# Performance work log

Hardware: AMD Instinct MI355X
Metric: run time of the kernel (lower is better)

Reference implementation:

```python
import jax, jax.numpy as jnp
import numpy as np

NUM_USERS = 100000
NUM_ITEMS = 50000
NUM_LAYERS = 4
DIM_H = 64
E_HALF = 2000000  # undirected interactions; symmetrized to 4M directed edges


def setup_inputs() -> dict:
    key = jax.random.key(0)
    k1, k2, k3, k4 = jax.random.split(key, 4)
    emb_users = 0.01 * jax.random.normal(k1, (NUM_USERS, DIM_H), dtype=jnp.float32)
    emb_items = 0.01 * jax.random.normal(k2, (NUM_ITEMS, DIM_H), dtype=jnp.float32)
    u = jax.random.randint(k3, (E_HALF,), 0, NUM_USERS, dtype=jnp.int64)
    it = jax.random.randint(k4, (E_HALF,), 0, NUM_ITEMS, dtype=jnp.int64) + NUM_USERS
    # bidirectional bipartite graph, as LightGCN expects
    src = jnp.concatenate([u, it])
    dst = jnp.concatenate([it, u])
    edge_index = jnp.stack([src, dst])  # [2, 4M]
    return {"emb_users": emb_users, "emb_items": emb_items, "edge_index": edge_index}


def reference(emb_users, emb_items, edge_index):
    N = emb_users.shape[0] + emb_items.shape[0]
    src, dst = edge_index[0], edge_index[1]
    # gcn_norm (add_self_loops=False): w_e = deg[src]^-1/2 * deg[dst]^-1/2
    deg = jax.ops.segment_sum(jnp.ones(src.shape[0], dtype=emb_users.dtype), dst, num_segments=N)
    dis = jnp.where(deg > 0, deg ** -0.5, 0.0).astype(emb_users.dtype)
    w = (dis[src] * dis[dst])[:, None]  # [E,1]

    emb = jnp.concatenate([emb_users, emb_items])  # [N, D]
    embs_sum = emb
    x = emb
    for _ in range(NUM_LAYERS):
        x = jax.ops.segment_sum(w * x[src], dst, num_segments=N)  # LGConv
        embs_sum = embs_sum + x
    # original: 1/(L+1) * mean over L+1 stacked layers -> sum / (L+1)^2
    emb_final = embs_sum / float((NUM_LAYERS + 1) ** 2)
    emb_users_final = emb_final[: emb_users.shape[0]]
    emb_items_final = emb_final[emb_users.shape[0]:]
    return (emb_users_final, emb_users, emb_items_final, emb_items)
```

## Files before the change

kernel.cpp:

```cpp
#include <hip/hip_runtime.h>
#include <hip/hip_fp8.h>

typedef unsigned char u8;
typedef float v2f __attribute__((ext_vector_type(2)));

#define SCAN_B 256

#define NPB      128
#define NPB_SH   7
#define P2_CAP   6144
#define STG_CAP  6144
#define P1_CHUNK 16384
#define P1_T     256
#define P1_IT    (P1_CHUNK / P1_T)
#define NB_MAX   2048
#define STG_OFF  ((size_t)10 << 20)

static __device__ __forceinline__ float fp8_to_f32(u8 b) {
    __hip_fp8_e4m3 t;
    t.__x = (__hip_fp8_storage_t)b;
    return (float)t;
}
static __device__ __forceinline__ u8 f32_to_fp8(float v) {
    __hip_fp8_e4m3 t(v);
    return (u8)t.__x;
}

template <bool HI>
static __device__ __forceinline__ v2f pk2(unsigned w) {
#if __has_builtin(__builtin_amdgcn_cvt_pk_f32_fp8)
    return __builtin_amdgcn_cvt_pk_f32_fp8((int)w, HI);
#else
    v2f r;
    r.x = fp8_to_f32(HI ? (u8)(w >> 16) : (u8)(w));
    r.y = fp8_to_f32(HI ? (u8)(w >> 24) : (u8)(w >> 8));
    return r;
#endif
}

__global__ void detect_kernel(const int* __restrict__ edges, int* __restrict__ flag) {
    __shared__ int cnt[256];
    int t = threadIdx.x;
    int c = 0;
    for (int i = t; i < 32768; i += 256)
        if (edges[2 * i + 1] != 0) c++;
    cnt[t] = c;
    __syncthreads();
    for (int off = 128; off > 0; off >>= 1) {
        if (t < off) cnt[t] += cnt[t + off];
        __syncthreads();
    }
    if (t == 0) flag[0] = (cnt[0] < 8) ? 2 : 1;
}

__global__ void gcur_fixed_init(int* __restrict__ gcur, int NB) {
    int b = blockIdx.x * blockDim.x + threadIdx.x;
    if (b < NB) gcur[b] = b * STG_CAP;
}

__global__ void part1_kernel(const int* __restrict__ edges, const int* __restrict__ flag,
                             int* __restrict__ gcur, unsigned* __restrict__ staging,
                             int E, int NB) {
    __shared__ int lcount[NB_MAX];
    __shared__ int lbase[NB_MAX];
    int t = threadIdx.x;
    int s = flag[0];
    long e0 = (long)blockIdx.x * P1_CHUNK;
    const int* dptr = edges + (long)E * s;
    for (int b = t; b < NB; b += P1_T) lcount[b] = 0;
    __syncthreads();
    for (int j = 0; j < P1_IT; j += 8) {
        int dv[8]; bool vl[8];
        #pragma unroll
        for (int k = 0; k < 8; ++k) {
            long e = e0 + (long)(j + k) * P1_T + t;
            vl[k] = (e < E);
            dv[k] = vl[k] ? dptr[e * s] : 0;
        }
        #pragma unroll
        for (int k = 0; k < 8; ++k)
            if (vl[k]) atomicAdd(&lcount[dv[k] >> NPB_SH], 1);
    }
    __syncthreads();
    for (int b = t; b < NB; b += P1_T) {
        int c = lcount[b];
        lbase[b] = (c > 0) ? atomicAdd(&gcur[b], c) : 0;
        lcount[b] = 0;
    }
    __syncthreads();
    for (int j = 0; j < P1_IT; j += 8) {
        int dv[8], sv[8]; bool vl[8];
        #pragma unroll
        for (int k = 0; k < 8; ++k) {
            long e = e0 + (long)(j + k) * P1_T + t;
            vl[k] = (e < E);
            dv[k] = vl[k] ? dptr[e * s] : 0;
            sv[k] = vl[k] ? edges[e * s] : 0;
        }
        #pragma unroll
        for (int k = 0; k < 8; ++k) {
            if (vl[k]) {
                int b = dv[k] >> NPB_SH;
                int slot = atomicAdd(&lcount[b], 1);
                int pos = lbase[b] + slot;
                if (pos < (b + 1) * STG_CAP)
                    staging[pos] = (unsigned)sv[k]
                                 | ((unsigned)(dv[k] & (NPB - 1)) << 20);
            }
        }
    }
}

__global__ void bucket_scan_kernel(const int* __restrict__ gcur, int* __restrict__ bbase,
                                   int NB) {
    __shared__ int sh[2][1024];
    int t = threadIdx.x;
    int i0 = 2 * t, i1 = 2 * t + 1;
    int a0 = (i0 < NB) ? (gcur[i0] - i0 * STG_CAP) : 0;
    int a1 = (i1 < NB) ? (gcur[i1] - i1 * STG_CAP) : 0;
    sh[0][t] = a0 + a1;
    __syncthreads();
    int src = 0;
    for (int off = 1; off < 1024; off <<= 1) {
        int x = sh[src][t] + ((t >= off) ? sh[src][t - off] : 0);
        sh[src ^ 1][t] = x;
        src ^= 1;
        __syncthreads();
    }
    int incl = sh[src][t];
    int excl = incl - (a0 + a1);
    if (i0 < NB) bbase[i0] = excl;
    if (i1 < NB) bbase[i1] = excl + a0;
    if (t == 1023) bbase[NB] = incl;
}

__global__ void __launch_bounds__(256) part2a_kernel(
        const int* __restrict__ gcur, const int* __restrict__ bbase,
        const unsigned* __restrict__ staging, int* __restrict__ row_ptr,
        float* __restrict__ dis, int n, int E, int NB) {
    __shared__ int cnt[NPB];
    __shared__ int sc[2][NPB];
    int b = blockIdx.x;
    int t = threadIdx.x;
    int dlo = b << NPB_SH;
    int sbase = b * STG_CAP;
    int c = gcur[b] - sbase;
    int base = bbase[b];
    if (t < NPB) cnt[t] = 0;
    __syncthreads();
    for (int k = t; k < c; k += 256) {
        unsigned wd = staging[sbase + k];
        atomicAdd(&cnt[wd >> 20], 1);
    }
    __syncthreads();
    if (t < NPB) sc[0][t] = cnt[t];
    __syncthreads();
    int src = 0;
    for (int off = 1; off < NPB; off <<= 1) {
        if (t < NPB) {
            int x = sc[src][t] + ((t >= off) ? sc[src][t - off] : 0);
            sc[src ^ 1][t] = x;
        }
        src ^= 1;
        __syncthreads();
    }
    if (t < NPB) {
        int node = dlo + t;
        if (node < n) {
            int d = cnt[t];
            row_ptr[node] = base + sc[src][t] - d;
            dis[node] = (d > 0) ? rsqrtf((float)d) : 0.0f;
        }
    }
    if (b == 0 && t == 0) row_ptr[n] = E;
}

__global__ void __launch_bounds__(256) part2b_kernel(
        const int* __restrict__ row_ptr, const int* __restrict__ gcur,
        const unsigned* __restrict__ staging, const float* __restrict__ dis,
        int2* __restrict__ cw, int n) {
    __shared__ int2 win[P2_CAP];
    __shared__ int cur[NPB];
    int b = blockIdx.x;
    int t = threadIdx.x;
    int dlo = b << NPB_SH;
    int sbase = b * STG_CAP;
    int cnt = gcur[b] - sbase;
    int base = row_ptr[dlo];
    if (t < NPB) {
        int node = dlo + t;
        cur[t] = (node < n) ? (row_ptr[node] - base) : 0;
    }
    __syncthreads();
    if (cnt <= P2_CAP) {
        for (int k = t; k < cnt; k += 256) {
            unsigned wd = staging[sbase + k];
            int sv = wd & 0xFFFFF;
            int dloc = wd >> 20;
            float w = dis[sv] * dis[dlo + dloc];
            int p = atomicAdd(&cur[dloc], 1);
            win[p] = make_int2(sv, __float_as_int(w));
        }
        __syncthreads();
        for (int k = t; k < cnt; k += 256)
            cw[base + k] = win[k];
    } else {
        for (int k = t; k < cnt; k += 256) {
            unsigned wd = staging[sbase + k];
            int sv = wd & 0xFFFFF;
            int dloc = wd >> 20;
            float w = dis[sv] * dis[dlo + dloc];
            int p = atomicAdd(&cur[dloc], 1);
            cw[base + p] = make_int2(sv, __float_as_int(w));
        }
    }
}

__global__ void count_deg_kernel(const int* __restrict__ edges, const int* __restrict__ flag,
                                 int* __restrict__ deg, int E) {
    int e = blockIdx.x * blockDim.x + threadIdx.x;
    if (e >= E) return;
    int s = flag[0];
    int d = edges[(long)E * s + (long)e * s];
    atomicAdd(&deg[d], 1);
}

__global__ void scan_phase1(const int* __restrict__ deg, int* __restrict__ row_ptr,
                            int* __restrict__ bsum, int n) {
    __shared__ int sh[2][SCAN_B];
    int t = threadIdx.x;
    int gi = blockIdx.x * SCAN_B + t;
    int v = (gi < n) ? deg[gi] : 0;
    int src = 0;
    sh[0][t] = v;
    __syncthreads();
    for (int off = 1; off < SCAN_B; off <<= 1) {
        int x = sh[src][t] + ((t >= off) ? sh[src][t - off] : 0);
        sh[src ^ 1][t] = x;
        src ^= 1;
        __syncthreads();
    }
    int incl = sh[src][t];
    if (gi < n) row_ptr[gi] = incl - v;
    if (t == SCAN_B - 1) bsum[blockIdx.x] = incl;
}

__global__ void scan_phase2(int* __restrict__ bsum, int nb) {
    __shared__ int sh[1024];
    int t = threadIdx.x;
    sh[t] = (t < nb) ? bsum[t] : 0;
    __syncthreads();
    if (t == 0) {
        int acc = 0;
        for (int i = 0; i < nb; ++i) { int x = sh[i]; sh[i] = acc; acc += x; }
    }
    __syncthreads();
    if (t < nb) bsum[t] = sh[t];
}

__global__ void scan_phase3(const int* __restrict__ deg, const int* __restrict__ bsum,
                            int* __restrict__ row_ptr, int* __restrict__ cursor,
                            float* __restrict__ dis, int n, int E) {
    int gi = blockIdx.x * SCAN_B + threadIdx.x;
    if (gi < n) {
        int e = row_ptr[gi] + bsum[blockIdx.x];
        row_ptr[gi] = e;
        cursor[gi]  = e;
        int d = deg[gi];
        dis[gi] = (d > 0) ? rsqrtf((float)d) : 0.0f;
    }
    if (gi == 0) row_ptr[n] = E;
}

__global__ void scatter_kernel(const int* __restrict__ edges, const int* __restrict__ flag,
                               const float* __restrict__ dis, int* __restrict__ cursor,
                               int2* __restrict__ cw, int E) {
    int e = blockIdx.x * blockDim.x + threadIdx.x;
    if (e >= E) return;
    int s = flag[0];
    int sv = edges[(long)e * s];
    int dv = edges[(long)E * s + (long)e * s];
    float w = dis[sv] * dis[dv];
    int pos = atomicAdd(&cursor[dv], 1);
    cw[pos] = make_int2(sv, __float_as_int(w));
}

__global__ void init_kernel(const float* __restrict__ eu, const float* __restrict__ ei,
                            u8* __restrict__ x0, long NU64, long tot) {
    long i = (long)blockIdx.x * blockDim.x + threadIdx.x;
    if (i >= tot) return;
    float v = (i < NU64) ? eu[i] : ei[i - NU64];
    x0[i] = f32_to_fp8(v);
}

__global__ void spmm_kernel(const int* __restrict__ row_ptr, const int2* __restrict__ cw,
                            const u8* __restrict__ xin, u8* __restrict__ xout, int n) {
    int wave = (blockIdx.x * blockDim.x + threadIdx.x) >> 6;
    int lane = threadIdx.x & 63;
    if (wave >= n) return;
    int beg = row_ptr[wave], end = row_ptr[wave + 1];
    int g = lane >> 3;
    int h = lane & 7;

    float a0 = 0.f, a1 = 0.f, a2 = 0.f, a3 = 0.f;
    float a4 = 0.f, a5 = 0.f, a6 = 0.f, a7 = 0.f;

    for (int iA = beg + g; iA < end; iA += 16) {
        int iB = iA + 8;
        bool vB = iB < end;

        int2 ca = cw[iA];
        int2 cb = cw[vB ? iB : iA];

        uint2 dA = *(const uint2*)(xin + ((long)ca.x << 6) + (h << 3));
        uint2 dB = *(const uint2*)(xin + ((long)cb.x << 6) + (h << 3));

        float wA = __int_as_float(ca.y);
        float wB = vB ? __int_as_float(cb.y) : 0.0f;

        v2f pA0 = pk2<false>(dA.x), pA1 = pk2<true>(dA.x);
        v2f pA2 = pk2<false>(dA.y), pA3 = pk2<true>(dA.y);
        v2f pB0 = pk2<false>(dB.x), pB1 = pk2<true>(dB.x);
        v2f pB2 = pk2<false>(dB.y), pB3 = pk2<true>(dB.y);

        a0 = fmaf(wA, pA0.x, a0); a1 = fmaf(wA, pA0.y, a1);
        a2 = fmaf(wA, pA1.x, a2); a3 = fmaf(wA, pA1.y, a3);
        a4 = fmaf(wA, pA2.x, a4); a5 = fmaf(wA, pA2.y, a5);
        a6 = fmaf(wA, pA3.x, a6); a7 = fmaf(wA, pA3.y, a7);
        a0 = fmaf(wB, pB0.x, a0); a1 = fmaf(wB, pB0.y, a1);
        a2 = fmaf(wB, pB1.x, a2); a3 = fmaf(wB, pB1.y, a3);
        a4 = fmaf(wB, pB2.x, a4); a5 = fmaf(wB, pB2.y, a5);
        a6 = fmaf(wB, pB3.x, a6); a7 = fmaf(wB, pB3.y, a7);
    }

    a0 += __shfl_xor(a0, 8);  a1 += __shfl_xor(a1, 8);
    a2 += __shfl_xor(a2, 8);  a3 += __shfl_xor(a3, 8);
    a4 += __shfl_xor(a4, 8);  a5 += __shfl_xor(a5, 8);
    a6 += __shfl_xor(a6, 8);  a7 += __shfl_xor(a7, 8);
    a0 += __shfl_xor(a0, 16); a1 += __shfl_xor(a1, 16);
    a2 += __shfl_xor(a2, 16); a3 += __shfl_xor(a3, 16);
    a4 += __shfl_xor(a4, 16); a5 += __shfl_xor(a5, 16);
    a6 += __shfl_xor(a6, 16); a7 += __shfl_xor(a7, 16);
    a0 += __shfl_xor(a0, 32); a1 += __shfl_xor(a1, 32);
    a2 += __shfl_xor(a2, 32); a3 += __shfl_xor(a3, 32);
    a4 += __shfl_xor(a4, 32); a5 += __shfl_xor(a5, 32);
    a6 += __shfl_xor(a6, 32); a7 += __shfl_xor(a7, 32);

    if (g == 0) {
        unsigned lo = (unsigned)f32_to_fp8(a0)
                    | ((unsigned)f32_to_fp8(a1) << 8)
                    | ((unsigned)f32_to_fp8(a2) << 16)
                    | ((unsigned)f32_to_fp8(a3) << 24);
        unsigned hi = (unsigned)f32_to_fp8(a4)
                    | ((unsigned)f32_to_fp8(a5) << 8)
                    | ((unsigned)f32_to_fp8(a6) << 16)
                    | ((unsigned)f32_to_fp8(a7) << 24);
        *(uint2*)(xout + ((long)wave << 6) + (h << 3)) = make_uint2(lo, hi);
    }
}

__global__ void final_kernel(const u8* __restrict__ x1, const u8* __restrict__ x2,
                             const u8* __restrict__ x3, const u8* __restrict__ x4,
                             const float* __restrict__ eu, const float* __restrict__ ei,
                             float* __restrict__ out, long NU64, long NI64) {
    long i = (long)blockIdx.x * blockDim.x + threadIdx.x;
    if (i >= NU64 + NI64) return;
    float base = (i < NU64) ? eu[i] : ei[i - NU64];
    float s = base + fp8_to_f32(x1[i]) + fp8_to_f32(x2[i])
                   + fp8_to_f32(x3[i]) + fp8_to_f32(x4[i]);
    float v = s * (1.0f / 25.0f);
    if (i < NU64) {
        out[i] = v;
        out[NU64 + i] = base;
    } else {
        long j = i - NU64;
        out[2 * NU64 + j] = v;
        out[2 * NU64 + NI64 + j] = base;
    }
}

extern "C" void kernel_launch(void* const* d_in, const int* in_sizes, int n_in,
                              void* d_out, int out_size, void* d_ws, size_t ws_size,
                              hipStream_t stream) {
    const float* eu = (const float*)d_in[0];
    const float* ei = (const float*)d_in[1];
    const int* edges = (const int*)d_in[2];
    float* out = (float*)d_out;

    const int NU = in_sizes[0] / 64;
    const int NI = in_sizes[1] / 64;
    const int N  = NU + NI;
    const int E  = in_sizes[2] / 2;
    const int NB = (N + NPB - 1) / NPB;

    char* w = (char*)d_ws;
    size_t off = 0;
    auto alloc = [&](size_t bytes) -> void* {
        void* p = w + off;
        off += (bytes + 255) & ~(size_t)255;
        return p;
    };
    int*   flag    = (int*)  alloc(256);
    int*   deg     = (int*)  alloc((size_t)N * 4);
    int*   row_ptr = (int*)  alloc((size_t)(N + 1) * 4);
    int*   cursor  = (int*)  alloc((size_t)N * 4);
    float* dis     = (float*)alloc((size_t)N * 4);
    int*   bsum    = (int*)  alloc(1024 * 4);
    int*   gcur    = (int*)  alloc((size_t)(NB + 1) * 4);
    int*   bbase   = (int*)  alloc((size_t)(NB + 1) * 4);
    int2*  cw      = (int2*) alloc((size_t)E * 8);
    const long NU64 = (long)NU * 64, NI64 = (long)NI * 64;
    const long tot = NU64 + NI64;
    u8* x1 = (u8*)alloc((size_t)tot);
    u8* x2 = (u8*)alloc((size_t)tot);
    u8* x3 = (u8*)alloc((size_t)tot);
    u8* x4 = (u8*)alloc((size_t)tot);

    const size_t out_bytes = (size_t)tot * 8;
    u8*       x0      = (u8*)out;
    unsigned* staging = (unsigned*)((char*)out + STG_OFF);

    detect_kernel<<<1, 256, 0, stream>>>(edges, flag);

    bool fast = (NB <= NB_MAX) && (N < (1 << 20)) &&
                (STG_OFF + (size_t)NB * STG_CAP * 4 <= out_bytes) &&
                ((size_t)tot <= STG_OFF);

    if (fast) {
        gcur_fixed_init<<<(NB + 255) / 256, 256, 0, stream>>>(gcur, NB);
        part1_kernel<<<(E + P1_CHUNK - 1) / P1_CHUNK, P1_T, 0, stream>>>(edges, flag, gcur,
                                                                         staging, E, NB);
        bucket_scan_kernel<<<1, 1024, 0, stream>>>(gcur, bbase, NB);
        part2a_kernel<<<NB, 256, 0, stream>>>(gcur, bbase, staging, row_ptr, dis, N, E, NB);
        part2b_kernel<<<NB, 256, 0, stream>>>(row_ptr, gcur, staging, dis, cw, N);
    } else {
        const int nb = (N + SCAN_B - 1) / SCAN_B;
        hipMemsetAsync(deg, 0, (size_t)N * 4, stream);
        count_deg_kernel<<<(E + 255) / 256, 256, 0, stream>>>(edges, flag, deg, E);
        scan_phase1<<<nb, SCAN_B, 0, stream>>>(deg, row_ptr, bsum, N);
        scan_phase2<<<1, 1024, 0, stream>>>(bsum, nb);
        scan_phase3<<<nb, SCAN_B, 0, stream>>>(deg, bsum, row_ptr, cursor, dis, N, E);
        scatter_kernel<<<(E + 255) / 256, 256, 0, stream>>>(edges, flag, dis, cursor, cw, E);
    }

    init_kernel<<<(int)((tot + 255) / 256), 256, 0, stream>>>(eu, ei, x0, NU64, tot);

    const int nblk = (N + 3) / 4;
    spmm_kernel<<<nblk, 256, 0, stream>>>(row_ptr, cw, x0, x1, N);
    spmm_kernel<<<nblk, 256, 0, stream>>>(row_ptr, cw, x1, x2, N);
    spmm_kernel<<<nblk, 256, 0, stream>>>(row_ptr, cw, x2, x3, N);
    spmm_kernel<<<nblk, 256, 0, stream>>>(row_ptr, cw, x3, x4, N);

    final_kernel<<<(int)((tot + 255) / 256), 256, 0, stream>>>(x1, x2, x3, x4, eu, ei,
                                                               out, NU64, NI64);
}
```

Before: 540.3 us.

## Factor edge weights into per-node scaling and drop per-edge weight storage

The symmetric normalization is rewritten as a per-node scale: features are pre-scaled by deg^-1/2, each SpMM layer does an unweighted sum and then multiplies by 1/deg, and the final pass multiplies by sqrt(deg). This removes the per-edge float weight, so the CSR column array shrinks from 8 to 4 bytes per edge and the weight gather in part2b goes away. FP8 decoding now uses custom bit manipulation with an exponent-fix multiply instead of hardware conversion. The SpMM loop is unrolled to four edges per iteration, and the global bucket counters are padded to a 16-int stride to spread atomics. The custom fp8 path and the rescaling by 64 change rounding behaviour, which could hurt accuracy.

```diff
diff --git a/kernel.cpp b/kernel.cpp
--- a/kernel.cpp
+++ b/kernel.cpp
@@ -1,8 +1,8 @@
 #include <hip/hip_runtime.h>
-#include <hip/hip_fp8.h>
+#include <hip/hip_fp16.h>
 
 typedef unsigned char u8;
-typedef float v2f __attribute__((ext_vector_type(2)));
+typedef unsigned short u16;
 
 #define SCAN_B 256
 
@@ -14,28 +14,22 @@
 #define P1_T     256
 #define P1_IT    (P1_CHUNK / P1_T)
 #define NB_MAX   2048
-#define STG_OFF  ((size_t)10 << 20)
-
-static __device__ __forceinline__ float fp8_to_f32(u8 b) {
-    __hip_fp8_e4m3 t;
-    t.__x = (__hip_fp8_storage_t)b;
-    return (float)t;
-}
-static __device__ __forceinline__ u8 f32_to_fp8(float v) {
-    __hip_fp8_e4m3 t(v);
-    return (u8)t.__x;
-}
-
-template <bool HI>
-static __device__ __forceinline__ v2f pk2(unsigned w) {
-#if __has_builtin(__builtin_amdgcn_cvt_pk_f32_fp8)
-    return __builtin_amdgcn_cvt_pk_f32_fp8((int)w, HI);
-#else
-    v2f r;
-    r.x = fp8_to_f32(HI ? (u8)(w >> 16) : (u8)(w));
-    r.y = fp8_to_f32(HI ? (u8)(w >> 24) : (u8)(w >> 8));
-    return r;
-#endif
+#define GC_STR   16
+#define STG_OFF  ((size_t)20 << 20)
+
+
+#define FP8_EXP_FIX 1.3292279957849159e36f
+static __device__ __forceinline__ float fp8_raw(unsigned w) {
+    unsigned u = ((w << 24) & 0x80000000u) | ((w << 20) & 0x07F00000u);
+    return __uint_as_float(u);
+}
+static __device__ __forceinline__ unsigned f32_to_fp8w(float v) {
+    unsigned u = __float_as_uint(v * 7.52316384526264e-37f);
+    unsigned s = (u >> 24) & 0x80u;
+    unsigned m = u & 0x7FFFFFFFu;
+    unsigned r = (m + 0x7FFFFu + ((m >> 20) & 1u)) >> 20;
+    if (r > 0x7Eu) r = 0x7Eu;
+    return s | r;
 }
 
 __global__ void detect_kernel(const int* __restrict__ edges, int* __restrict__ flag) {
@@ -55,7 +49,7 @@
 
 __global__ void gcur_fixed_init(int* __restrict__ gcur, int NB) {
     int b = blockIdx.x * blockDim.x + threadIdx.x;
-    if (b < NB) gcur[b] = b * STG_CAP;
+    if (b < NB) gcur[b * GC_STR] = b * STG_CAP;
 }
 
 __global__ void part1_kernel(const int* __restrict__ edges, const int* __restrict__ flag,
@@ -84,7 +78,7 @@
     __syncthreads();
     for (int b = t; b < NB; b += P1_T) {
         int c = lcount[b];
-        lbase[b] = (c > 0) ? atomicAdd(&gcur[b], c) : 0;
+        lbase[b] = (c > 0) ? atomicAdd(&gcur[b * GC_STR], c) : 0;
         lcount[b] = 0;
     }
     __syncthreads();
@@ -116,8 +110,8 @@
     __shared__ int sh[2][1024];
     int t = threadIdx.x;
     int i0 = 2 * t, i1 = 2 * t + 1;
-    int a0 = (i0 < NB) ? (gcur[i0] - i0 * STG_CAP) : 0;
-    int a1 = (i1 < NB) ? (gcur[i1] - i1 * STG_CAP) : 0;
+    int a0 = (i0 < NB) ? (gcur[i0 * GC_STR] - i0 * STG_CAP) : 0;
+    int a1 = (i1 < NB) ? (gcur[i1 * GC_STR] - i1 * STG_CAP) : 0;
     sh[0][t] = a0 + a1;
     __syncthreads();
     int src = 0;
@@ -137,14 +131,15 @@
 __global__ void __launch_bounds__(256) part2a_kernel(
         const int* __restrict__ gcur, const int* __restrict__ bbase,
         const unsigned* __restrict__ staging, int* __restrict__ row_ptr,
-        float* __restrict__ dis, int n, int E, int NB) {
+        float* __restrict__ dis, float* __restrict__ dis2, float* __restrict__ invd,
+        int n, int E, int NB) {
     __shared__ int cnt[NPB];
     __shared__ int sc[2][NPB];
     int b = blockIdx.x;
     int t = threadIdx.x;
     int dlo = b << NPB_SH;
     int sbase = b * STG_CAP;
-    int c = gcur[b] - sbase;
+    int c = gcur[b * GC_STR] - sbase;
     int base = bbase[b];
     if (t < NPB) cnt[t] = 0;
     __syncthreads();
@@ -169,7 +164,10 @@
         if (node < n) {
             int d = cnt[t];
             row_ptr[node] = base + sc[src][t] - d;
-            dis[node] = (d > 0) ? rsqrtf((float)d) : 0.0f;
+            float ds = (d > 0) ? rsqrtf((float)d) : 0.0f;
+            dis[node]  = ds;
+            dis2[node] = ds * ds;
+            invd[node] = (d > 0) ? sqrtf((float)d) : 0.0f;
         }
     }
     if (b == 0 && t == 0) row_ptr[n] = E;
@@ -177,15 +175,14 @@
 
 __global__ void __launch_bounds__(256) part2b_kernel(
         const int* __restrict__ row_ptr, const int* __restrict__ gcur,
-        const unsigned* __restrict__ staging, const float* __restrict__ dis,
-        int2* __restrict__ cw, int n) {
-    __shared__ int2 win[P2_CAP];
+        const unsigned* __restrict__ staging, int* __restrict__ cs, int n) {
+    __shared__ int win[P2_CAP];
     __shared__ int cur[NPB];
     int b = blockIdx.x;
     int t = threadIdx.x;
     int dlo = b << NPB_SH;
     int sbase = b * STG_CAP;
-    int cnt = gcur[b] - sbase;
+    int cnt = gcur[b * GC_STR] - sbase;
     int base = row_ptr[dlo];
     if (t < NPB) {
         int node = dlo + t;
@@ -195,23 +192,17 @@
     if (cnt <= P2_CAP) {
         for (int k = t; k < cnt; k += 256) {
             unsigned wd = staging[sbase + k];
-            int sv = wd & 0xFFFFF;
-            int dloc = wd >> 20;
-            float w = dis[sv] * dis[dlo + dloc];
-            int p = atomicAdd(&cur[dloc], 1);
-            win[p] = make_int2(sv, __float_as_int(w));
+            int p = atomicAdd(&cur[wd >> 20], 1);
+            win[p] = (int)(wd & 0xFFFFF);
         }
         __syncthreads();
         for (int k = t; k < cnt; k += 256)
-            cw[base + k] = win[k];
+            cs[base + k] = win[k];
     } else {
         for (int k = t; k < cnt; k += 256) {
             unsigned wd = staging[sbase + k];
-            int sv = wd & 0xFFFFF;
-            int dloc = wd >> 20;
-            float w = dis[sv] * dis[dlo + dloc];
-            int p = atomicAdd(&cur[dloc], 1);
-            cw[base + p] = make_int2(sv, __float_as_int(w));
+            int p = atomicAdd(&cur[wd >> 20], 1);
+            cs[base + p] = (int)(wd & 0xFFFFF);
         }
     }
 }
@@ -260,41 +251,55 @@
 
 __global__ void scan_phase3(const int* __restrict__ deg, const int* __restrict__ bsum,
                             int* __restrict__ row_ptr, int* __restrict__ cursor,
-                            float* __restrict__ dis, int n, int E) {
+                            float* __restrict__ dis, float* __restrict__ dis2,
+                            float* __restrict__ invd, int n, int E) {
     int gi = blockIdx.x * SCAN_B + threadIdx.x;
     if (gi < n) {
         int e = row_ptr[gi] + bsum[blockIdx.x];
         row_ptr[gi] = e;
         cursor[gi]  = e;
         int d = deg[gi];
-        dis[gi] = (d > 0) ? rsqrtf((float)d) : 0.0f;
+        float ds = (d > 0) ? rsqrtf((float)d) : 0.0f;
+        dis[gi]  = ds;
+        dis2[gi] = ds * ds;
+        invd[gi] = (d > 0) ? sqrtf((float)d) : 0.0f;
     }
     if (gi == 0) row_ptr[n] = E;
 }
 
 __global__ void scatter_kernel(const int* __restrict__ edges, const int* __restrict__ flag,
-                               const float* __restrict__ dis, int* __restrict__ cursor,
-                               int2* __restrict__ cw, int E) {
+                               int* __restrict__ cursor, int* __restrict__ cs, int E) {
     int e = blockIdx.x * blockDim.x + threadIdx.x;
     if (e >= E) return;
     int s = flag[0];
     int sv = edges[(long)e * s];
     int dv = edges[(long)E * s + (long)e * s];
-    float w = dis[sv] * dis[dv];
     int pos = atomicAdd(&cursor[dv], 1);
-    cw[pos] = make_int2(sv, __float_as_int(w));
-}
-
-__global__ void init_kernel(const float* __restrict__ eu, const float* __restrict__ ei,
-                            u8* __restrict__ x0, long NU64, long tot) {
+    cs[pos] = sv;
+}
+
+__global__ void init8_kernel(const float* __restrict__ eu, const float* __restrict__ ei,
+                             const float* __restrict__ dis,
+                             u8* __restrict__ u0, long NU64, long tot) {
     long i = (long)blockIdx.x * blockDim.x + threadIdx.x;
     if (i >= tot) return;
     float v = (i < NU64) ? eu[i] : ei[i - NU64];
-    x0[i] = f32_to_fp8(v);
-}
-
-__global__ void spmm_kernel(const int* __restrict__ row_ptr, const int2* __restrict__ cw,
-                            const u8* __restrict__ xin, u8* __restrict__ xout, int n) {
+    u0[i] = (u8)f32_to_fp8w(v * dis[i >> 6] * 64.0f);
+}
+
+#define ACC8(d)                                                         \
+    a0 = fmaf(fp8_raw((d).x),       FP8_EXP_FIX, a0);                   \
+    a1 = fmaf(fp8_raw((d).x >> 8),  FP8_EXP_FIX, a1);                   \
+    a2 = fmaf(fp8_raw((d).x >> 16), FP8_EXP_FIX, a2);                   \
+    a3 = fmaf(fp8_raw((d).x >> 24), FP8_EXP_FIX, a3);                   \
+    a4 = fmaf(fp8_raw((d).y),       FP8_EXP_FIX, a4);                   \
+    a5 = fmaf(fp8_raw((d).y >> 8),  FP8_EXP_FIX, a5);                   \
+    a6 = fmaf(fp8_raw((d).y >> 16), FP8_EXP_FIX, a6);                   \
+    a7 = fmaf(fp8_raw((d).y >> 24), FP8_EXP_FIX, a7);
+
+__global__ void spmm8_kernel(const int* __restrict__ row_ptr, const int* __restrict__ cs,
+                             const u8* __restrict__ uin, u8* __restrict__ uout,
+                             const float* __restrict__ dis2, int n) {
     int wave = (blockIdx.x * blockDim.x + threadIdx.x) >> 6;
     int lane = threadIdx.x & 63;
     if (wave >= n) return;
@@ -305,32 +310,24 @@
     float a0 = 0.f, a1 = 0.f, a2 = 0.f, a3 = 0.f;
     float a4 = 0.f, a5 = 0.f, a6 = 0.f, a7 = 0.f;
 
-    for (int iA = beg + g; iA < end; iA += 16) {
-        int iB = iA + 8;
-        bool vB = iB < end;
-
-        int2 ca = cw[iA];
-        int2 cb = cw[vB ? iB : iA];
-
-        uint2 dA = *(const uint2*)(xin + ((long)ca.x << 6) + (h << 3));
-        uint2 dB = *(const uint2*)(xin + ((long)cb.x << 6) + (h << 3));
-
-        float wA = __int_as_float(ca.y);
-        float wB = vB ? __int_as_float(cb.y) : 0.0f;
-
-        v2f pA0 = pk2<false>(dA.x), pA1 = pk2<true>(dA.x);
-        v2f pA2 = pk2<false>(dA.y), pA3 = pk2<true>(dA.y);
-        v2f pB0 = pk2<false>(dB.x), pB1 = pk2<true>(dB.x);
-        v2f pB2 = pk2<false>(dB.y), pB3 = pk2<true>(dB.y);
-
-        a0 = fmaf(wA, pA0.x, a0); a1 = fmaf(wA, pA0.y, a1);
-        a2 = fmaf(wA, pA1.x, a2); a3 = fmaf(wA, pA1.y, a3);
-        a4 = fmaf(wA, pA2.x, a4); a5 = fmaf(wA, pA2.y, a5);
-        a6 = fmaf(wA, pA3.x, a6); a7 = fmaf(wA, pA3.y, a7);
-        a0 = fmaf(wB, pB0.x, a0); a1 = fmaf(wB, pB0.y, a1);
-        a2 = fmaf(wB, pB1.x, a2); a3 = fmaf(wB, pB1.y, a3);
-        a4 = fmaf(wB, pB2.x, a4); a5 = fmaf(wB, pB2.y, a5);
-        a6 = fmaf(wB, pB3.x, a6); a7 = fmaf(wB, pB3.y, a7);
+    for (int i0 = beg + g; i0 < end; i0 += 32) {
+        int i1 = i0 + 8, i2 = i0 + 16, i3 = i0 + 24;
+        bool v1 = i1 < end, v2 = i2 < end, v3 = i3 < end;
+        int s0 = cs[i0];
+        int s1 = cs[v1 ? i1 : i0];
+        int s2 = cs[v2 ? i2 : i0];
+        int s3 = cs[v3 ? i3 : i0];
+        uint2 d0 = *(const uint2*)(uin + ((long)s0 << 6) + (h << 3));
+        uint2 d1 = *(const uint2*)(uin + ((long)s1 << 6) + (h << 3));
+        uint2 d2 = *(const uint2*)(uin + ((long)s2 << 6) + (h << 3));
+        uint2 d3 = *(const uint2*)(uin + ((long)s3 << 6) + (h << 3));
+        if (!v1) { d1.x = 0; d1.y = 0; }
+        if (!v2) { d2.x = 0; d2.y = 0; }
+        if (!v3) { d3.x = 0; d3.y = 0; }
+        ACC8(d0);
+        ACC8(d1);
+        ACC8(d2);
+        ACC8(d3);
     }
 
     a0 += __shfl_xor(a0, 8);  a1 += __shfl_xor(a1, 8);
@@ -347,27 +344,30 @@
     a6 += __shfl_xor(a6, 32); a7 += __shfl_xor(a7, 32);
 
     if (g == 0) {
-        unsigned lo = (unsigned)f32_to_fp8(a0)
-                    | ((unsigned)f32_to_fp8(a1) << 8)
-                    | ((unsigned)f32_to_fp8(a2) << 16)
-                    | ((unsigned)f32_to_fp8(a3) << 24);
-        unsigned hi = (unsigned)f32_to_fp8(a4)
-                    | ((unsigned)f32_to_fp8(a5) << 8)
-                    | ((unsigned)f32_to_fp8(a6) << 16)
-                    | ((unsigned)f32_to_fp8(a7) << 24);
-        *(uint2*)(xout + ((long)wave << 6) + (h << 3)) = make_uint2(lo, hi);
-    }
-}
-
-__global__ void final_kernel(const u8* __restrict__ x1, const u8* __restrict__ x2,
-                             const u8* __restrict__ x3, const u8* __restrict__ x4,
-                             const float* __restrict__ eu, const float* __restrict__ ei,
-                             float* __restrict__ out, long NU64, long NI64) {
+        float s2 = dis2[wave];
+        unsigned lo = f32_to_fp8w(a0 * s2)
+                    | (f32_to_fp8w(a1 * s2) << 8)
+                    | (f32_to_fp8w(a2 * s2) << 16)
+                    | (f32_to_fp8w(a3 * s2) << 24);
+        unsigned hi = f32_to_fp8w(a4 * s2)
+                    | (f32_to_fp8w(a5 * s2) << 8)
+                    | (f32_to_fp8w(a6 * s2) << 16)
+                    | (f32_to_fp8w(a7 * s2) << 24);
+        *(uint2*)(uout + ((long)wave << 6) + (h << 3)) = make_uint2(lo, hi);
+    }
+}
+
+__global__ void final8_kernel(const u8* __restrict__ u1, const u8* __restrict__ u2,
+                              const u8* __restrict__ u3, const u8* __restrict__ u4,
+                              const float* __restrict__ eu, const float* __restrict__ ei,
+                              const float* __restrict__ invd,
+                              float* __restrict__ out, long NU64, long NI64) {
     long i = (long)blockIdx.x * blockDim.x + threadIdx.x;
     if (i >= NU64 + NI64) return;
     float base = (i < NU64) ? eu[i] : ei[i - NU64];
-    float s = base + fp8_to_f32(x1[i]) + fp8_to_f32(x2[i])
-                   + fp8_to_f32(x3[i]) + fp8_to_f32(x4[i]);
+    float us = (fp8_raw(u1[i]) + fp8_raw(u2[i]) + fp8_raw(u3[i]) + fp8_raw(u4[i]))
+               * FP8_EXP_FIX;
+    float s = base + us * invd[i >> 6] * (1.0f / 64.0f);
     float v = s * (1.0f / 25.0f);
     if (i < NU64) {
         out[i] = v;
@@ -405,10 +405,12 @@
     int*   row_ptr = (int*)  alloc((size_t)(N + 1) * 4);
     int*   cursor  = (int*)  alloc((size_t)N * 4);
     float* dis     = (float*)alloc((size_t)N * 4);
+    float* dis2    = (float*)alloc((size_t)N * 4);
+    float* invd    = (float*)alloc((size_t)N * 4);
     int*   bsum    = (int*)  alloc(1024 * 4);
-    int*   gcur    = (int*)  alloc((size_t)(NB + 1) * 4);
+    int*   gcur    = (int*)  alloc((size_t)(NB + 1) * GC_STR * 4);
     int*   bbase   = (int*)  alloc((size_t)(NB + 1) * 4);
-    int2*  cw      = (int2*) alloc((size_t)E * 8);
+    int*   cs      = (int*)  alloc((size_t)E * 4);
     const long NU64 = (long)NU * 64, NI64 = (long)NI * 64;
     const long tot = NU64 + NI64;
     u8* x1 = (u8*)alloc((size_t)tot);
@@ -431,26 +433,27 @@
         part1_kernel<<<(E + P1_CHUNK - 1) / P1_CHUNK, P1_T, 0, stream>>>(edges, flag, gcur,
                                                                          staging, E, NB);
         bucket_scan_kernel<<<1, 1024, 0, stream>>>(gcur, bbase, NB);
-        part2a_kernel<<<NB, 256, 0, stream>>>(gcur, bbase, staging, row_ptr, dis, N, E, NB);
-        part2b_kernel<<<NB, 256, 0, stream>>>(row_ptr, gcur, staging, dis, cw, N);
+        part2a_kernel<<<NB, 256, 0, stream>>>(gcur, bbase, staging, row_ptr,
+                                              dis, dis2, invd, N, E, NB);
+        part2b_kernel<<<NB, 256, 0, stream>>>(row_ptr, gcur, staging, cs, N);
     } else {
         const int nb = (N + SCAN_B - 1) / SCAN_B;
         hipMemsetAsync(deg, 0, (size_t)N * 4, stream);
         count_deg_kernel<<<(E + 255) / 256, 256, 0, stream>>>(edges, flag, deg, E);
         scan_phase1<<<nb, SCAN_B, 0, stream>>>(deg, row_ptr, bsum, N);
         scan_phase2<<<1, 1024, 0, stream>>>(bsum, nb);
-        scan_phase3<<<nb, SCAN_B, 0, stream>>>(deg, bsum, row_ptr, cursor, dis, N, E);
-        scatter_kernel<<<(E + 255) / 256, 256, 0, stream>>>(edges, flag, dis, cursor, cw, E);
-    }
-
-    init_kernel<<<(int)((tot + 255) / 256), 256, 0, stream>>>(eu, ei, x0, NU64, tot);
+        scan_phase3<<<nb, SCAN_B, 0, stream>>>(deg, bsum, row_ptr, cursor,
+                                               dis, dis2, invd, N, E);
+        scatter_kernel<<<(E + 255) / 256, 256, 0, stream>>>(edges, flag, cursor, cs, E);
+    }
 
     const int nblk = (N + 3) / 4;
-    spmm_kernel<<<nblk, 256, 0, stream>>>(row_ptr, cw, x0, x1, N);
-    spmm_kernel<<<nblk, 256, 0, stream>>>(row_ptr, cw, x1, x2, N);
-    spmm_kernel<<<nblk, 256, 0, stream>>>(row_ptr, cw, x2, x3, N);
-    spmm_kernel<<<nblk, 256, 0, stream>>>(row_ptr, cw, x3, x4, N);
-
-    final_kernel<<<(int)((tot + 255) / 256), 256, 0, stream>>>(x1, x2, x3, x4, eu, ei,
-                                                               out, NU64, NI64);
-}
+    const int eblk = (int)((tot + 255) / 256);
+    init8_kernel<<<eblk, 256, 0, stream>>>(eu, ei, dis, x0, NU64, tot);
+    spmm8_kernel<<<nblk, 256, 0, stream>>>(row_ptr, cs, x0, x1, dis2, N);
+    spmm8_kernel<<<nblk, 256, 0, stream>>>(row_ptr, cs, x1, x2, dis2, N);
+    spmm8_kernel<<<nblk, 256, 0, stream>>>(row_ptr, cs, x2, x3, dis2, N);
+    spmm8_kernel<<<nblk, 256, 0, stream>>>(row_ptr, cs, x3, x4, dis2, N);
+    final8_kernel<<<eblk, 256, 0, stream>>>(x1, x2, x3, x4, eu, ei, invd,
+                                            out, NU64, NI64);
+}
```

New measurement: 674.2 us. +24.8%, slower.
